# Kernel optimization log

Measured on AMD Instinct MI355X. Metric: run time of the kernel, lower is better.

## Reference

```python
import jax, jax.numpy as jnp
import numpy as np

LARGE_NUMBER = 1.0e10
B, NV, H = 512, 48, 32


def setup_inputs() -> dict:
    key = jax.random.key(0)
    k_z, k_wc, k_bc, k_wy, k_by, k_m = jax.random.split(key, 6)
    z = jax.random.normal(k_z, (B * NV, H), dtype=jnp.float32)
    Wc = jax.random.normal(k_wc, (H, H), dtype=jnp.float32) * 0.05
    bc = jax.random.normal(k_bc, (H,), dtype=jnp.float32) * 0.05
    Wy = jax.random.normal(k_wy, (H, H), dtype=jnp.float32) * 0.05
    by = jax.random.normal(k_by, (H,), dtype=jnp.float32) * 0.05
    mask = (jax.random.uniform(k_m, (B * NV, 1)) > 0.3).astype(jnp.int32)
    return {"z": z, "Wc": Wc, "bc": bc, "Wy": Wy, "by": by,
            "mask": mask, "num_graphs": B, "nv": NV}


def reference(z, Wc, bc, Wy, by, mask, num_graphs, nv):
    # Faithful translation of Attention.forward (sigmoid-gated pairwise node attention).
    # torch.nn.Linear(x) == x @ W.T + b; applying Linear after tiling == tiling after Linear.
    h = Wc.shape[0]
    m = mask.reshape(num_graphs, nv, 1).astype(z.dtype)            # (B, nv, 1)
    zc = (z @ Wc.T + bc).reshape(num_graphs, nv, h)                 # lin_attention_c
    zy = (z @ Wy.T + by).reshape(num_graphs, nv, h)                 # lin_attention_y
    # atten_mask_c + atten_mask_yi = (m_i + m_j)*L - 2L, broadcast over H
    mask_add = (m[:, :, None, :] + m[:, None, :, :]) * LARGE_NUMBER - 2.0 * LARGE_NUMBER
    s = jax.nn.sigmoid(zc[:, :, None, :] + zy[:, None, :, :] + mask_add)  # (B, nv, nv, H)
    denom = jnp.sum(m, axis=1, keepdims=True)                       # (B, 1, 1) valid-node count
    atten_mi = jnp.sum(s, axis=2) / denom                           # (B, nv, H)
    return atten_mi.reshape(-1, h)
```

## Files before the change

kernel.cpp:

```cpp
#include <hip/hip_runtime.h>


#define LOG2E 1.4426950408889634f

constexpr int NV = 48;
constexpr int H  = 32;
constexpr int BLOCK = 512;
constexpr int WPAD = 36;
constexpr float F_INV = 1.0e8f;

__global__ __launch_bounds__(BLOCK, 4)
void OptLinker_attn_kernel(const float* __restrict__ z,
                           const float* __restrict__ Wc,
                           const float* __restrict__ bc,
                           const float* __restrict__ Wy,
                           const float* __restrict__ by,
                           const int*   __restrict__ mask,
                           float* __restrict__ out)
{
    __shared__ float z_s[NV * H];
    __shared__ float F_s[NV * H];
    __shared__ float wc_s[H * WPAD];
    __shared__ float wy_s[H * WPAD];

    const int b   = blockIdx.x;
    const int tid = threadIdx.x;
    const int h   = tid & 31;
    const int i0  = tid >> 5;

    const float4* zb4 = (const float4*)(z + (size_t)b * (NV * H));
    if (tid < (NV * H) / 4) ((float4*)z_s)[tid] = zb4[tid];

    {
        const int q = tid & 255;
        const float4 v = (tid < 256) ? ((const float4*)Wc)[q]
                                     : ((const float4*)Wy)[q];
        float* dst = (tid < 256 ? wc_s : wy_s) + (q >> 3) * WPAD + (q & 7) * 4;
        *(float4*)dst = v;
    }

    const int lane = tid & 63;
    const int mv = (lane < NV) ? mask[b * NV + lane] : 0;
    const unsigned long long bits = __ballot(mv != 0);
    const float bcv = bc[h], byv = by[h];

    __syncthreads();

    float4 wc_r[8], wy_r[8];
    {
        const float* wrc = wc_s + h * WPAD;
        const float* wry = wy_s + h * WPAD;
        #pragma unroll
        for (int q = 0; q < 8; ++q) {
            wc_r[q] = *(const float4*)(wrc + q * 4);
            wy_r[q] = *(const float4*)(wry + q * 4);
        }
    }

    float E[3];
    #pragma unroll
    for (int it = 0; it < 3; ++it) {
        const int i = i0 + it * 16;
        float accC = bcv, accY = byv;
        const float4* zr = (const float4*)(z_s + i * H);
        #pragma unroll
        for (int q = 0; q < 8; ++q) {
            const float4 zv = zr[q];
            accC = fmaf(zv.x, wc_r[q].x, accC);
            accC = fmaf(zv.y, wc_r[q].y, accC);
            accC = fmaf(zv.z, wc_r[q].z, accC);
            accC = fmaf(zv.w, wc_r[q].w, accC);
            accY = fmaf(zv.x, wy_r[q].x, accY);
            accY = fmaf(zv.y, wy_r[q].y, accY);
            accY = fmaf(zv.z, wy_r[q].z, accY);
            accY = fmaf(zv.w, wy_r[q].w, accY);
        }
        E[it] = __builtin_amdgcn_exp2f(-accC * LOG2E);
        const bool vi = (bits >> i) & 1ull;
        F_s[i * H + h] = vi ? __builtin_amdgcn_exp2f(-accY * LOG2E) : F_INV;
    }
    __syncthreads();

    float acc[3] = {0.f, 0.f, 0.f};
    #pragma unroll
    for (int j = 0; j < NV; j += 4) {
        const float f0 = F_s[(j + 0) * H + h];
        const float f1 = F_s[(j + 1) * H + h];
        const float f2 = F_s[(j + 2) * H + h];
        const float f3 = F_s[(j + 3) * H + h];
        #pragma unroll
        for (int it = 0; it < 3; ++it) {
            const float Ei = E[it];
            const float t0 = fmaf(Ei, f0, 1.0f);
            const float t1 = fmaf(Ei, f1, 1.0f);
            const float t2 = fmaf(Ei, f2, 1.0f);
            const float t3 = fmaf(Ei, f3, 1.0f);
            const float p01 = t0 * t1, p23 = t2 * t3;
            const float den = p01 * p23;
            const float num = fmaf(t0 + t1, p23, (t2 + t3) * p01);
            acc[it] = fmaf(num, __builtin_amdgcn_rcpf(den), acc[it]);
        }
    }

    const int nvalid = __popcll(bits);
    const float rden = __builtin_amdgcn_rcpf((float)nvalid);
    float* ob = out + (size_t)b * (NV * H);
    #pragma unroll
    for (int it = 0; it < 3; ++it) {
        const int i = i0 + it * 16;
        ob[i * H + h] = ((bits >> i) & 1ull) ? acc[it] * rden : 0.0f;
    }
}

extern "C" void kernel_launch(void* const* d_in, const int* in_sizes, int n_in,
                              void* d_out, int out_size, void* d_ws, size_t ws_size,
                              hipStream_t stream) {
    const float* z    = (const float*)d_in[0];
    const float* Wc   = (const float*)d_in[1];
    const float* bc   = (const float*)d_in[2];
    const float* Wy   = (const float*)d_in[3];
    const float* by   = (const float*)d_in[4];
    const int*   mask = (const int*)d_in[5];
    float* out = (float*)d_out;

    const int ngraph = in_sizes[0] / (NV * H);
    OptLinker_attn_kernel<<<ngraph, BLOCK, 0, stream>>>(z, Wc, bc, Wy, by, mask, out);
}
```

Before: 11.32 us.

## Compact valid nodes per graph and skip masked rows and columns

Builds a per-graph index of valid nodes using a ballot prefix count, then computes projections and pairwise sigmoid sums only over the compacted valid set. The j loop runs over ceil(nvalid/4) groups, with F_INV padding rows filling the tail. The third row group is skipped when it holds no valid node. This cuts the pairwise work in proportion to the mask density, in exchange for data-dependent loop bounds, an indirect scatter on output, and extra shared-memory index traffic.

```diff
diff --git a/kernel.cpp b/kernel.cpp
--- a/kernel.cpp
+++ b/kernel.cpp
@@ -7,6 +7,7 @@
 constexpr int H  = 32;
 constexpr int BLOCK = 512;
 constexpr int WPAD = 36;
+constexpr int FROWS = 52;
 constexpr float F_INV = 1.0e8f;
 
 __global__ __launch_bounds__(BLOCK, 4)
@@ -19,14 +20,19 @@
                            float* __restrict__ out)
 {
     __shared__ float z_s[NV * H];
-    __shared__ float F_s[NV * H];
+    __shared__ float F_s[FROWS * H];
     __shared__ float wc_s[H * WPAD];
     __shared__ float wy_s[H * WPAD];
+    __shared__ int   validIdx[NV];
 
     const int b   = blockIdx.x;
     const int tid = threadIdx.x;
     const int h   = tid & 31;
     const int i0  = tid >> 5;
+
+    const int lane = tid & 63;
+    const int mv = (lane < NV) ? mask[b * NV + lane] : 0;
+    const float bcv = bc[h], byv = by[h];
 
     const float4* zb4 = (const float4*)(z + (size_t)b * (NV * H));
     if (tid < (NV * H) / 4) ((float4*)z_s)[tid] = zb4[tid];
@@ -39,10 +45,18 @@
         *(float4*)dst = v;
     }
 
-    const int lane = tid & 63;
-    const int mv = (lane < NV) ? mask[b * NV + lane] : 0;
     const unsigned long long bits = __ballot(mv != 0);
-    const float bcv = bc[h], byv = by[h];
+    const int nvalid = __popcll(bits);
+
+    if (tid < NV) validIdx[tid] = 0;
+    if (tid < 64 && mv != 0) {
+        const int pos = __popcll(bits & ((1ull << lane) - 1ull));
+        validIdx[pos] = lane;
+    }
+    if (tid < 4 * H) {
+        const int r = nvalid + (tid >> 5);
+        if (r < FROWS) F_s[r * H + h] = F_INV;
+    }
 
     __syncthreads();
 
@@ -57,12 +71,10 @@
         }
     }
 
-    float E[3];
-    #pragma unroll
-    for (int it = 0; it < 3; ++it) {
-        const int i = i0 + it * 16;
+    auto stageA = [&](int v, float& Eout) {
+        const int r = validIdx[v];
         float accC = bcv, accY = byv;
-        const float4* zr = (const float4*)(z_s + i * H);
+        const float4* zr = (const float4*)(z_s + r * H);
         #pragma unroll
         for (int q = 0; q < 8; ++q) {
             const float4 zv = zr[q];
@@ -75,41 +87,67 @@
             accY = fmaf(zv.z, wy_r[q].z, accY);
             accY = fmaf(zv.w, wy_r[q].w, accY);
         }
-        E[it] = __builtin_amdgcn_exp2f(-accC * LOG2E);
-        const bool vi = (bits >> i) & 1ull;
-        F_s[i * H + h] = vi ? __builtin_amdgcn_exp2f(-accY * LOG2E) : F_INV;
-    }
+        Eout = __builtin_amdgcn_exp2f(-accC * LOG2E);
+        if (v < nvalid)
+            F_s[v * H + h] = __builtin_amdgcn_exp2f(-accY * LOG2E);
+    };
+
+    float E0, E1, E2 = 0.f;
+    const bool hasRow2 = (i0 + 32) < nvalid;
+    stageA(i0, E0);
+    stageA(i0 + 16, E1);
+    if (hasRow2) stageA(i0 + 32, E2);
+
     __syncthreads();
 
-    float acc[3] = {0.f, 0.f, 0.f};
-    #pragma unroll
-    for (int j = 0; j < NV; j += 4) {
-        const float f0 = F_s[(j + 0) * H + h];
-        const float f1 = F_s[(j + 1) * H + h];
-        const float f2 = F_s[(j + 2) * H + h];
-        const float f3 = F_s[(j + 3) * H + h];
-        #pragma unroll
-        for (int it = 0; it < 3; ++it) {
-            const float Ei = E[it];
-            const float t0 = fmaf(Ei, f0, 1.0f);
-            const float t1 = fmaf(Ei, f1, 1.0f);
-            const float t2 = fmaf(Ei, f2, 1.0f);
-            const float t3 = fmaf(Ei, f3, 1.0f);
+    const int nq = (nvalid + 3) >> 2;
+    float acc0 = 0.f, acc1 = 0.f, acc2 = 0.f;
+    #pragma unroll 2
+    for (int q = 0; q < nq; ++q) {
+        const float f0 = F_s[(4 * q + 0) * H + h];
+        const float f1 = F_s[(4 * q + 1) * H + h];
+        const float f2 = F_s[(4 * q + 2) * H + h];
+        const float f3 = F_s[(4 * q + 3) * H + h];
+        {
+            const float t0 = fmaf(E0, f0, 1.0f), t1 = fmaf(E0, f1, 1.0f);
+            const float t2 = fmaf(E0, f2, 1.0f), t3 = fmaf(E0, f3, 1.0f);
             const float p01 = t0 * t1, p23 = t2 * t3;
-            const float den = p01 * p23;
             const float num = fmaf(t0 + t1, p23, (t2 + t3) * p01);
-            acc[it] = fmaf(num, __builtin_amdgcn_rcpf(den), acc[it]);
+            acc0 = fmaf(num, __builtin_amdgcn_rcpf(p01 * p23), acc0);
+        }
+        {
+            const float t0 = fmaf(E1, f0, 1.0f), t1 = fmaf(E1, f1, 1.0f);
+            const float t2 = fmaf(E1, f2, 1.0f), t3 = fmaf(E1, f3, 1.0f);
+            const float p01 = t0 * t1, p23 = t2 * t3;
+            const float num = fmaf(t0 + t1, p23, (t2 + t3) * p01);
+            acc1 = fmaf(num, __builtin_amdgcn_rcpf(p01 * p23), acc1);
+        }
+    }
+    if (hasRow2) {
+        #pragma unroll 2
+        for (int q = 0; q < nq; ++q) {
+            const float f0 = F_s[(4 * q + 0) * H + h];
+            const float f1 = F_s[(4 * q + 1) * H + h];
+            const float f2 = F_s[(4 * q + 2) * H + h];
+            const float f3 = F_s[(4 * q + 3) * H + h];
+            const float t0 = fmaf(E2, f0, 1.0f), t1 = fmaf(E2, f1, 1.0f);
+            const float t2 = fmaf(E2, f2, 1.0f), t3 = fmaf(E2, f3, 1.0f);
+            const float p01 = t0 * t1, p23 = t2 * t3;
+            const float num = fmaf(t0 + t1, p23, (t2 + t3) * p01);
+            acc2 = fmaf(num, __builtin_amdgcn_rcpf(p01 * p23), acc2);
         }
     }
 
-    const int nvalid = __popcll(bits);
     const float rden = __builtin_amdgcn_rcpf((float)nvalid);
     float* ob = out + (size_t)b * (NV * H);
     #pragma unroll
     for (int it = 0; it < 3; ++it) {
         const int i = i0 + it * 16;
-        ob[i * H + h] = ((bits >> i) & 1ull) ? acc[it] * rden : 0.0f;
+        if (!((bits >> i) & 1ull)) ob[i * H + h] = 0.0f;
     }
+    if (i0 < nvalid)        ob[validIdx[i0] * H + h]      = acc0 * rden;
+    if (i0 + 16 < nvalid)   ob[validIdx[i0 + 16] * H + h] = acc1 * rden;
+    if (hasRow2)            ob[validIdx[i0 + 32] * H + h] = acc2 * rden;
 }
 
 extern "C" void kernel_launch(void* const* d_in, const int* in_sizes, int n_in,
```

Result: slower. 18.90 us (+66.9%).
